# Kernel tuning notes

Measured on AMD Instinct MI355X. Metric: run time of the kernel, lower is better.

## Reference

```python
import jax, jax.numpy as jnp
import numpy as np

B, T, D, BOT = 4, 4096, 2048, 256


def setup_inputs() -> dict:
    key = jax.random.key(0)
    k1, k2, k3, k4 = jax.random.split(key, 4)
    return {
        "hdc_chars": jax.random.normal(k1, (B, T, D), dtype=jnp.float32),
        "decay_matrix": jax.random.uniform(k2, (B, T, T), dtype=jnp.float32),
        "Wq": jax.random.normal(k3, (BOT, D), dtype=jnp.float32) * (D ** -0.5),
        "bq": jnp.zeros((BOT,), dtype=jnp.float32),
        "Wk": jax.random.normal(k4, (BOT, D), dtype=jnp.float32) * (D ** -0.5),
        "bk": jnp.zeros((BOT,), dtype=jnp.float32),
    }


def reference(hdc_chars, decay_matrix, Wq, bq, Wk, bk):
    # hdc_chars: [B,T,D]; decay_matrix: [B,T,T]
    bot = Wq.shape[0]
    scale = bot ** -0.5
    q = hdc_chars @ Wq.T + bq          # [B,T,bot]
    k = hdc_chars @ Wk.T + bk          # [B,T,bot]
    scores = jnp.einsum("btc,bsc->bts", q, k) * scale  # [B,T,T]
    t = scores.shape[-1]
    i = jnp.arange(t)[:, None]
    j = jnp.arange(t)[None, :]
    allowed = j <= i - 4               # tril(diagonal=-4): blocks local echo
    scores = jnp.where(allowed, scores, jnp.float32(-65000.0))
    resonance = jax.nn.softmax(scores, axis=-1)
    combined = 0.7 * decay_matrix + 0.3 * resonance
    return combined @ hdc_chars        # [B,T,D]
```

## Files before the change

### kernel.cpp

```cpp
#include <hip/hip_runtime.h>
#include <hip/hip_bf16.h>

#define BB 4
#define TT 4096
#define DD 2048
#define BOTC 256

typedef __bf16 bf16;
typedef __attribute__((ext_vector_type(8))) __bf16 bf16x8;
typedef __attribute__((ext_vector_type(4))) float f32x4;

constexpr int BM = 128, BN = 128, BK = 32;

__device__ __forceinline__ void async16(const void* g, bf16* l) {
  __builtin_amdgcn_global_load_lds((const __attribute__((address_space(1))) void*)g,
                                   (__attribute__((address_space(3))) void*)l, 16, 0, 0);
}

template <int EPI>
__global__ __launch_bounds__(256) void gemm_bt(
    const bf16* __restrict__ A, const bf16* __restrict__ Bm, void* __restrict__ Cout,
    const float* __restrict__ bias, int M, int N, int K,
    long sAb, long sBb, long sCb, float scale) {
  const int b = blockIdx.z;
  const int m0 = blockIdx.y * BM;
  const int n0 = blockIdx.x * BN;
  const int tid = threadIdx.x;
  const int lane = tid & 63;
  const int w = tid >> 6;
  const int wm = (w >> 1) * 64;
  const int wn = (w & 1) * 64;

  if (EPI == 2 && n0 > m0) {
    bf16* C = (bf16*)Cout + (size_t)b * sCb;
    bf16 neg = (bf16)(-65000.0f);
    bf16x8 v8 = {neg, neg, neg, neg, neg, neg, neg, neg};
#pragma unroll
    for (int it = 0; it < 8; ++it) {
      int c = it * 256 + tid;
      int row = c >> 4, cc = c & 15;
      *(bf16x8*)(C + (size_t)(m0 + row) * N + n0 + cc * 8) = v8;
    }
    return;
  }

  __shared__ bf16 As[BM * BK];
  __shared__ bf16 Bs[BN * BK];

  f32x4 acc[4][4] = {};

  const bf16* Arow = A + (size_t)b * sAb + (size_t)m0 * K;
  const bf16* Brow = Bm + (size_t)b * sBb + (size_t)n0 * K;

  for (int k0 = 0; k0 < K; k0 += BK) {
#pragma unroll
    for (int j = 0; j < 2; ++j) {
      int c = j * 256 + tid;
      int row = c >> 2, kc = c & 3;
      async16(Arow + (size_t)row * K + k0 + kc * 8, As + c * 8);
      async16(Brow + (size_t)row * K + k0 + kc * 8, Bs + c * 8);
    }
    __syncthreads();
    bf16x8 af[4], bfr[4];
#pragma unroll
    for (int mi = 0; mi < 4; ++mi)
      af[mi] = *(const bf16x8*)(As + (wm + mi * 16 + (lane & 15)) * BK + (lane >> 4) * 8);
#pragma unroll
    for (int ni = 0; ni < 4; ++ni)
      bfr[ni] = *(const bf16x8*)(Bs + (wn + ni * 16 + (lane & 15)) * BK + (lane >> 4) * 8);
#pragma unroll
    for (int mi = 0; mi < 4; ++mi)
#pragma unroll
      for (int ni = 0; ni < 4; ++ni)
        acc[mi][ni] = __builtin_amdgcn_mfma_f32_16x16x32_bf16(af[mi], bfr[ni], acc[mi][ni], 0, 0, 0);
    __syncthreads();
  }

  const int lcol = lane & 15;
  const int lrow = (lane >> 4) * 4;

  if (EPI == 0) {
    float* C = (float*)Cout + (size_t)b * sCb;
#pragma unroll
    for (int mi = 0; mi < 4; ++mi) {
      int rbase = m0 + wm + mi * 16 + lrow;
#pragma unroll
      for (int ni = 0; ni < 4; ++ni) {
        int col = n0 + wn + ni * 16 + lcol;
#pragma unroll
        for (int r = 0; r < 4; ++r)
          C[(size_t)(rbase + r) * N + col] = acc[mi][ni][r];
      }
    }
  } else if (EPI == 1) {
    bf16* C = (bf16*)Cout + (size_t)b * sCb;
#pragma unroll
    for (int mi = 0; mi < 4; ++mi) {
      int rbase = m0 + wm + mi * 16 + lrow;
#pragma unroll
      for (int ni = 0; ni < 4; ++ni) {
        int col = n0 + wn + ni * 16 + lcol;
        float bv = bias[col];
#pragma unroll
        for (int r = 0; r < 4; ++r)
          C[(size_t)(rbase + r) * N + col] = (bf16)(acc[mi][ni][r] + bv);
      }
    }
  } else {
    bf16* C = (bf16*)Cout + (size_t)b * sCb;
#pragma unroll
    for (int mi = 0; mi < 4; ++mi) {
      int rbase = m0 + wm + mi * 16 + lrow;
#pragma unroll
      for (int ni = 0; ni < 4; ++ni) {
        int col = n0 + wn + ni * 16 + lcol;
#pragma unroll
        for (int r = 0; r < 4; ++r) {
          int i = rbase + r;
          float v = acc[mi][ni][r] * scale;
          if (col > i - 4) v = -65000.0f;
          C[(size_t)i * N + col] = (bf16)v;
        }
      }
    }
  }
}

__global__ __launch_bounds__(256) void conv_transpose(
    const float* __restrict__ hdc, bf16* __restrict__ hb, bf16* __restrict__ hT) {
  __shared__ float tile[32][33];
  int b = blockIdx.z;
  int d0 = blockIdx.x * 32, t0 = blockIdx.y * 32;
  int tx = threadIdx.x, ty = threadIdx.y;
  const float* src = hdc + (size_t)b * TT * DD;
  bf16* dstb = hb + (size_t)b * TT * DD;
  bf16* dstT = hT + (size_t)b * DD * TT;
#pragma unroll
  for (int rr = 0; rr < 32; rr += 8) {
    int r = ty + rr;
    float v = src[(size_t)(t0 + r) * DD + d0 + tx];
    tile[r][tx] = v;
    dstb[(size_t)(t0 + r) * DD + d0 + tx] = (bf16)v;
  }
  __syncthreads();
#pragma unroll
  for (int rr = 0; rr < 32; rr += 8) {
    int r = ty + rr;
    dstT[(size_t)(d0 + r) * TT + t0 + tx] = (bf16)tile[tx][r];
  }
}

__global__ __launch_bounds__(256) void conv_w(
    const float* __restrict__ Wq, const float* __restrict__ Wk,
    bf16* __restrict__ Wqb, bf16* __restrict__ Wkb) {
  int i = blockIdx.x * 256 + threadIdx.x;
  Wqb[i] = (bf16)Wq[i];
  Wkb[i] = (bf16)Wk[i];
}

__global__ __launch_bounds__(256) void softmax_combine(
    bf16* __restrict__ S, const float* __restrict__ decay) {
  int b = blockIdx.y, i = blockIdx.x;
  bf16* srow = S + ((size_t)b * TT + i) * TT;
  const float* drow = decay + ((size_t)b * TT + i) * TT;
  int t = threadIdx.x;
  int lane = t & 63, w = t >> 6;

  bf16x8 sv0 = *(const bf16x8*)(srow + (size_t)t * 8);
  bf16x8 sv1 = *(const bf16x8*)(srow + (size_t)(256 + t) * 8);
  float s[16];
#pragma unroll
  for (int e = 0; e < 8; ++e) { s[e] = (float)sv0[e]; s[8 + e] = (float)sv1[e]; }

  float m = s[0];
#pragma unroll
  for (int u = 1; u < 16; ++u) m = fmaxf(m, s[u]);
#pragma unroll
  for (int off = 32; off > 0; off >>= 1) m = fmaxf(m, __shfl_xor(m, off));
  __shared__ float redm[4], reds[4];
  if (lane == 0) redm[w] = m;
  __syncthreads();
  m = fmaxf(fmaxf(redm[0], redm[1]), fmaxf(redm[2], redm[3]));

  float p[16], sum = 0.f;
#pragma unroll
  for (int u = 0; u < 16; ++u) { p[u] = __expf(s[u] - m); sum += p[u]; }
#pragma unroll
  for (int off = 32; off > 0; off >>= 1) sum += __shfl_xor(sum, off);
  if (lane == 0) reds[w] = sum;
  __syncthreads();
  sum = reds[0] + reds[1] + reds[2] + reds[3];
  float inv = 0.3f / sum;

#pragma unroll
  for (int u = 0; u < 2; ++u) {
    int chunk = u * 256 + t;
    const float4* d4 = (const float4*)(drow + (size_t)chunk * 8);
    float4 da = d4[0], db = d4[1];
    bf16x8 o;
    o[0] = (bf16)(0.7f * da.x + p[u * 8 + 0] * inv);
    o[1] = (bf16)(0.7f * da.y + p[u * 8 + 1] * inv);
    o[2] = (bf16)(0.7f * da.z + p[u * 8 + 2] * inv);
    o[3] = (bf16)(0.7f * da.w + p[u * 8 + 3] * inv);
    o[4] = (bf16)(0.7f * db.x + p[u * 8 + 4] * inv);
    o[5] = (bf16)(0.7f * db.y + p[u * 8 + 5] * inv);
    o[6] = (bf16)(0.7f * db.z + p[u * 8 + 6] * inv);
    o[7] = (bf16)(0.7f * db.w + p[u * 8 + 7] * inv);
    *(bf16x8*)(srow + (size_t)chunk * 8) = o;
  }
}

extern "C" void kernel_launch(void* const* d_in, const int* in_sizes, int n_in,
                              void* d_out, int out_size, void* d_ws, size_t ws_size,
                              hipStream_t stream) {
  (void)in_sizes; (void)n_in; (void)out_size; (void)ws_size;
  const float* hdc = (const float*)d_in[0];
  const float* decay = (const float*)d_in[1];
  const float* Wq = (const float*)d_in[2];
  const float* bq = (const float*)d_in[3];
  const float* Wk = (const float*)d_in[4];
  const float* bk = (const float*)d_in[5];
  float* out = (float*)d_out;

  char* ws = (char*)d_ws;
  bf16* hdc_b = (bf16*)ws; ws += (size_t)BB * TT * DD * 2;
  bf16* hdcT  = (bf16*)ws; ws += (size_t)BB * TT * DD * 2;
  bf16* Wqb   = (bf16*)ws; ws += (size_t)BOTC * DD * 2;
  bf16* Wkb   = (bf16*)ws; ws += (size_t)BOTC * DD * 2;
  bf16* qb    = (bf16*)ws; ws += (size_t)BB * TT * BOTC * 2;
  bf16* kb    = (bf16*)ws; ws += (size_t)BB * TT * BOTC * 2;
  bf16* S     = (bf16*)ws; ws += (size_t)BB * TT * TT * 2;

  conv_transpose<<<dim3(DD / 32, TT / 32, BB), dim3(32, 8), 0, stream>>>(hdc, hdc_b, hdcT);
  conv_w<<<dim3(BOTC * DD / 256), 256, 0, stream>>>(Wq, Wk, Wqb, Wkb);

  gemm_bt<1><<<dim3(BOTC / BN, (BB * TT) / BM, 1), 256, 0, stream>>>(
      hdc_b, Wqb, qb, bq, BB * TT, BOTC, DD, 0, 0, 0, 1.0f);
  gemm_bt<1><<<dim3(BOTC / BN, (BB * TT) / BM, 1), 256, 0, stream>>>(
      hdc_b, Wkb, kb, bk, BB * TT, BOTC, DD, 0, 0, 0, 1.0f);

  gemm_bt<2><<<dim3(TT / BN, TT / BM, BB), 256, 0, stream>>>(
      qb, kb, S, nullptr, TT, TT, BOTC,
      (long)TT * BOTC, (long)TT * BOTC, (long)TT * TT, 0.0625f);

  softmax_combine<<<dim3(TT, BB), 256, 0, stream>>>(S, decay);

  gemm_bt<0><<<dim3(DD / BN, TT / BM, BB), 256, 0, stream>>>(
      S, hdcT, out, nullptr, TT, DD, TT,
      (long)TT * TT, (long)DD * TT, (long)TT * DD, 1.0f);
}
```

Before: 1.070 ms.

## Widen GEMM K-tile with XOR-swizzled LDS, fuse QK projection, skip masked score work

The GEMM K tile grows from 32 to 64 and the LDS layout is XOR-swizzled so fragment reads avoid bank conflicts. The Q and K projections are merged into one GEMM over a concatenated weight and bias buffer, writing an interleaved qk tensor read with leading-dimension strides. The score kernel no longer writes the masked upper tiles, and the softmax reads only the valid prefix of each row, handling fully masked rows as uniform. The transpose and conversion kernels are vectorized with 64x64 tiles. The changes aim to cut LDS stalls, kernel launches and memory traffic, at the cost of more complex indexing and larger LDS use per block.

```diff
diff --git a/kernel.cpp b/kernel.cpp
--- a/kernel.cpp
+++ b/kernel.cpp
@@ -7,10 +7,11 @@
 #define BOTC 256
 
 typedef __bf16 bf16;
+typedef __attribute__((ext_vector_type(4))) __bf16 bf16x4;
 typedef __attribute__((ext_vector_type(8))) __bf16 bf16x8;
 typedef __attribute__((ext_vector_type(4))) float f32x4;
 
-constexpr int BM = 128, BN = 128, BK = 32;
+constexpr int BM = 128, BN = 128, BK = 64;
 
 __device__ __forceinline__ void async16(const void* g, bf16* l) {
   __builtin_amdgcn_global_load_lds((const __attribute__((address_space(1))) void*)g,
@@ -20,7 +21,7 @@
 template <int EPI>
 __global__ __launch_bounds__(256) void gemm_bt(
     const bf16* __restrict__ A, const bf16* __restrict__ Bm, void* __restrict__ Cout,
-    const float* __restrict__ bias, int M, int N, int K,
+    const float* __restrict__ bias, int M, int N, int K, int ldA, int ldB,
     long sAb, long sBb, long sCb, float scale) {
   const int b = blockIdx.z;
   const int m0 = blockIdx.y * BM;
@@ -31,48 +32,50 @@
   const int wm = (w >> 1) * 64;
   const int wn = (w & 1) * 64;
 
-  if (EPI == 2 && n0 > m0) {
-    bf16* C = (bf16*)Cout + (size_t)b * sCb;
-    bf16 neg = (bf16)(-65000.0f);
-    bf16x8 v8 = {neg, neg, neg, neg, neg, neg, neg, neg};
-#pragma unroll
-    for (int it = 0; it < 8; ++it) {
-      int c = it * 256 + tid;
-      int row = c >> 4, cc = c & 15;
-      *(bf16x8*)(C + (size_t)(m0 + row) * N + n0 + cc * 8) = v8;
-    }
-    return;
-  }
+  if (EPI == 2 && n0 > m0) return;
 
   __shared__ bf16 As[BM * BK];
   __shared__ bf16 Bs[BN * BK];
 
   f32x4 acc[4][4] = {};
 
-  const bf16* Arow = A + (size_t)b * sAb + (size_t)m0 * K;
-  const bf16* Brow = Bm + (size_t)b * sBb + (size_t)n0 * K;
+  const bf16* Arow = A + (size_t)b * sAb + (size_t)m0 * ldA;
+  const bf16* Brow = Bm + (size_t)b * sBb + (size_t)n0 * ldB;
 
   for (int k0 = 0; k0 < K; k0 += BK) {
 #pragma unroll
-    for (int j = 0; j < 2; ++j) {
+    for (int j = 0; j < 4; ++j) {
       int c = j * 256 + tid;
-      int row = c >> 2, kc = c & 3;
-      async16(Arow + (size_t)row * K + k0 + kc * 8, As + c * 8);
-      async16(Brow + (size_t)row * K + k0 + kc * 8, Bs + c * 8);
+      int row = c >> 3, kc = c & 7;
+      int gk = kc ^ (row & 7);
+      async16(Arow + (size_t)row * ldA + k0 + gk * 8, As + (size_t)c * 8);
+      async16(Brow + (size_t)row * ldB + k0 + gk * 8, Bs + (size_t)c * 8);
     }
     __syncthreads();
-    bf16x8 af[4], bfr[4];
+    bf16x8 af[4][2], bfr[4][2];
 #pragma unroll
     for (int mi = 0; mi < 4; ++mi)
-      af[mi] = *(const bf16x8*)(As + (wm + mi * 16 + (lane & 15)) * BK + (lane >> 4) * 8);
+#pragma unroll
+      for (int kk = 0; kk < 2; ++kk) {
+        int row = wm + mi * 16 + (lane & 15);
+        int kc = kk * 4 + (lane >> 4);
+        af[mi][kk] = *(const bf16x8*)(As + ((size_t)row * 8 + (kc ^ (row & 7))) * 8);
+      }
 #pragma unroll
     for (int ni = 0; ni < 4; ++ni)
-      bfr[ni] = *(const bf16x8*)(Bs + (wn + ni * 16 + (lane & 15)) * BK + (lane >> 4) * 8);
-#pragma unroll
-    for (int mi = 0; mi < 4; ++mi)
-#pragma unroll
-      for (int ni = 0; ni < 4; ++ni)
-        acc[mi][ni] = __builtin_amdgcn_mfma_f32_16x16x32_bf16(af[mi], bfr[ni], acc[mi][ni], 0, 0, 0);
+#pragma unroll
+      for (int kk = 0; kk < 2; ++kk) {
+        int row = wn + ni * 16 + (lane & 15);
+        int kc = kk * 4 + (lane >> 4);
+        bfr[ni][kk] = *(const bf16x8*)(Bs + ((size_t)row * 8 + (kc ^ (row & 7))) * 8);
+      }
+#pragma unroll
+    for (int kk = 0; kk < 2; ++kk)
+#pragma unroll
+      for (int mi = 0; mi < 4; ++mi)
+#pragma unroll
+        for (int ni = 0; ni < 4; ++ni)
+          acc[mi][ni] = __builtin_amdgcn_mfma_f32_16x16x32_bf16(af[mi][kk], bfr[ni][kk], acc[mi][ni], 0, 0, 0);
     __syncthreads();
   }
 
@@ -128,34 +131,54 @@
 
 __global__ __launch_bounds__(256) void conv_transpose(
     const float* __restrict__ hdc, bf16* __restrict__ hb, bf16* __restrict__ hT) {
-  __shared__ float tile[32][33];
+  __shared__ float tile[64][65];
   int b = blockIdx.z;
-  int d0 = blockIdx.x * 32, t0 = blockIdx.y * 32;
-  int tx = threadIdx.x, ty = threadIdx.y;
+  int d0 = blockIdx.x * 64, t0 = blockIdx.y * 64;
+  int tid = threadIdx.x;
   const float* src = hdc + (size_t)b * TT * DD;
   bf16* dstb = hb + (size_t)b * TT * DD;
   bf16* dstT = hT + (size_t)b * DD * TT;
-#pragma unroll
-  for (int rr = 0; rr < 32; rr += 8) {
-    int r = ty + rr;
-    float v = src[(size_t)(t0 + r) * DD + d0 + tx];
-    tile[r][tx] = v;
-    dstb[(size_t)(t0 + r) * DD + d0 + tx] = (bf16)v;
+  int c4 = tid & 15, r0 = tid >> 4;
+#pragma unroll
+  for (int rr = 0; rr < 4; ++rr) {
+    int r = rr * 16 + r0;
+    float4 v = *(const float4*)(src + (size_t)(t0 + r) * DD + d0 + c4 * 4);
+    tile[r][c4 * 4 + 0] = v.x;
+    tile[r][c4 * 4 + 1] = v.y;
+    tile[r][c4 * 4 + 2] = v.z;
+    tile[r][c4 * 4 + 3] = v.w;
+    bf16x4 o;
+    o[0] = (bf16)v.x; o[1] = (bf16)v.y; o[2] = (bf16)v.z; o[3] = (bf16)v.w;
+    *(bf16x4*)(dstb + (size_t)(t0 + r) * DD + d0 + c4 * 4) = o;
   }
   __syncthreads();
-#pragma unroll
-  for (int rr = 0; rr < 32; rr += 8) {
-    int r = ty + rr;
-    dstT[(size_t)(d0 + r) * TT + t0 + tx] = (bf16)tile[tx][r];
+  int tc = tid & 7, dr0 = tid >> 3;
+#pragma unroll
+  for (int rr = 0; rr < 2; ++rr) {
+    int dr = rr * 32 + dr0;
+    bf16x8 o;
+#pragma unroll
+    for (int e = 0; e < 8; ++e) o[e] = (bf16)tile[tc * 8 + e][dr];
+    *(bf16x8*)(dstT + (size_t)(d0 + dr) * TT + t0 + tc * 8) = o;
   }
 }
 
 __global__ __launch_bounds__(256) void conv_w(
     const float* __restrict__ Wq, const float* __restrict__ Wk,
-    bf16* __restrict__ Wqb, bf16* __restrict__ Wkb) {
+    const float* __restrict__ bq, const float* __restrict__ bk,
+    bf16* __restrict__ Wqkb, float* __restrict__ bqk) {
   int i = blockIdx.x * 256 + threadIdx.x;
-  Wqb[i] = (bf16)Wq[i];
-  Wkb[i] = (bf16)Wk[i];
+  float4 q = *(const float4*)(Wq + (size_t)i * 4);
+  float4 k = *(const float4*)(Wk + (size_t)i * 4);
+  bf16x4 qo, ko;
+  qo[0] = (bf16)q.x; qo[1] = (bf16)q.y; qo[2] = (bf16)q.z; qo[3] = (bf16)q.w;
+  ko[0] = (bf16)k.x; ko[1] = (bf16)k.y; ko[2] = (bf16)k.z; ko[3] = (bf16)k.w;
+  *(bf16x4*)(Wqkb + (size_t)i * 4) = qo;
+  *(bf16x4*)(Wqkb + (size_t)BOTC * DD + (size_t)i * 4) = ko;
+  if (blockIdx.x == 0) {
+    bqk[threadIdx.x] = bq[threadIdx.x];
+    bqk[256 + threadIdx.x] = bk[threadIdx.x];
+  }
 }
 
 __global__ __launch_bounds__(256) void softmax_combine(
@@ -165,48 +188,81 @@
   const float* drow = decay + ((size_t)b * TT + i) * TT;
   int t = threadIdx.x;
   int lane = t & 63, w = t >> 6;
-
-  bf16x8 sv0 = *(const bf16x8*)(srow + (size_t)t * 8);
-  bf16x8 sv1 = *(const bf16x8*)(srow + (size_t)(256 + t) * 8);
-  float s[16];
-#pragma unroll
-  for (int e = 0; e < 8; ++e) { s[e] = (float)sv0[e]; s[8 + e] = (float)sv1[e]; }
-
-  float m = s[0];
-#pragma unroll
-  for (int u = 1; u < 16; ++u) m = fmaxf(m, s[u]);
-#pragma unroll
-  for (int off = 32; off > 0; off >>= 1) m = fmaxf(m, __shfl_xor(m, off));
-  __shared__ float redm[4], reds[4];
-  if (lane == 0) redm[w] = m;
-  __syncthreads();
-  m = fmaxf(fmaxf(redm[0], redm[1]), fmaxf(redm[2], redm[3]));
-
-  float p[16], sum = 0.f;
-#pragma unroll
-  for (int u = 0; u < 16; ++u) { p[u] = __expf(s[u] - m); sum += p[u]; }
-#pragma unroll
-  for (int off = 32; off > 0; off >>= 1) sum += __shfl_xor(sum, off);
-  if (lane == 0) reds[w] = sum;
-  __syncthreads();
-  sum = reds[0] + reds[1] + reds[2] + reds[3];
-  float inv = 0.3f / sum;
+  const int valid = i - 3;
+  const int nc = valid > 0 ? (valid + 7) >> 3 : 0;
+
+  float p[2][8];
+  float inv = 0.f, pc = 0.f;
+
+  if (valid > 0) {
+    float s[2][8];
+#pragma unroll
+    for (int u = 0; u < 2; ++u) {
+      int c = u * 256 + t;
+      if (c < nc) {
+        bf16x8 sv = *(const bf16x8*)(srow + (size_t)c * 8);
+#pragma unroll
+        for (int e = 0; e < 8; ++e) {
+          int j = c * 8 + e;
+          s[u][e] = j < valid ? (float)sv[e] : -INFINITY;
+        }
+      } else {
+#pragma unroll
+        for (int e = 0; e < 8; ++e) s[u][e] = -INFINITY;
+      }
+    }
+    float m = s[0][0];
+#pragma unroll
+    for (int u = 0; u < 2; ++u)
+#pragma unroll
+      for (int e = 0; e < 8; ++e) m = fmaxf(m, s[u][e]);
+#pragma unroll
+    for (int off = 32; off > 0; off >>= 1) m = fmaxf(m, __shfl_xor(m, off));
+    __shared__ float redm[4], reds[4];
+    if (lane == 0) redm[w] = m;
+    __syncthreads();
+    m = fmaxf(fmaxf(redm[0], redm[1]), fmaxf(redm[2], redm[3]));
+
+    float sum = 0.f;
+#pragma unroll
+    for (int u = 0; u < 2; ++u)
+#pragma unroll
+      for (int e = 0; e < 8; ++e) {
+        p[u][e] = __expf(s[u][e] - m);
+        sum += p[u][e];
+      }
+#pragma unroll
+    for (int off = 32; off > 0; off >>= 1) sum += __shfl_xor(sum, off);
+    if (lane == 0) reds[w] = sum;
+    __syncthreads();
+    sum = reds[0] + reds[1] + reds[2] + reds[3];
+    inv = 0.3f / sum;
+  } else {
+    pc = 0.3f / 4096.0f;
+#pragma unroll
+    for (int u = 0; u < 2; ++u)
+#pragma unroll
+      for (int e = 0; e < 8; ++e) p[u][e] = 0.f;
+  }
 
 #pragma unroll
   for (int u = 0; u < 2; ++u) {
-    int chunk = u * 256 + t;
-    const float4* d4 = (const float4*)(drow + (size_t)chunk * 8);
+    int c = u * 256 + t;
+    const float4* d4 = (const float4*)(drow + (size_t)c * 8);
     float4 da = d4[0], db = d4[1];
+    float pv[8];
+#pragma unroll
+    for (int e = 0; e < 8; ++e) pv[e] = p[u][e] * inv + pc;
     bf16x8 o;
-    o[0] = (bf16)(0.7f * da.x + p[u * 8 + 0] * inv);
-    o[1] = (bf16)(0.7f * da.y + p[u * 8 + 1] * inv);
-    o[2] = (bf16)(0.7f * da.z + p[u * 8 + 2] * inv);
-    o[3] = (bf16)(0.7f * da.w + p[u * 8 + 3] * inv);
-    o[4] = (bf16)(0.7f * db.x + p[u * 8 + 4] * inv);
-    o[5] = (bf16)(0.7f * db.y + p[u * 8 + 5] * inv);
-    o[6] = (bf16)(0.7f * db.z + p[u * 8 + 6] * inv);
-    o[7] = (bf16)(0.7f * db.w + p[u * 8 + 7] * inv);
-    *(bf16x8*)(srow + (size_t)chunk * 8) = o;
+    o[0] = (bf16)(0.7f * da.x + pv[0]);
+    o[1] = (bf16)(0.7f * da.y + pv[1]);
+    o[2] = (bf16)(0.7f * da.z + pv[2]);
+    o[3] = (bf16)(0.7f * da.w + pv[3]);
+    o[4] = (bf16)(0.7f * db.x + pv[4]);
+    o[5] = (bf16)(0.7f * db.y + pv[5]);
+    o[6] = (bf16)(0.7f * db.z + pv[6]);
+    o[7] = (bf16)(0.7f * db.w + pv[7]);
+    *(bf16x8*)(srow + (size_t)c * 8) = o;
   }
 }
 
@@ -225,27 +281,24 @@
   char* ws = (char*)d_ws;
   bf16* hdc_b = (bf16*)ws; ws += (size_t)BB * TT * DD * 2;
   bf16* hdcT  = (bf16*)ws; ws += (size_t)BB * TT * DD * 2;
-  bf16* Wqb   = (bf16*)ws; ws += (size_t)BOTC * DD * 2;
-  bf16* Wkb   = (bf16*)ws; ws += (size_t)BOTC * DD * 2;
-  bf16* qb    = (bf16*)ws; ws += (size_t)BB * TT * BOTC * 2;
-  bf16* kb    = (bf16*)ws; ws += (size_t)BB * TT * BOTC * 2;
+  bf16* Wqkb  = (bf16*)ws; ws += (size_t)2 * BOTC * DD * 2;
+  float* bqk  = (float*)ws; ws += 2 * BOTC * 4;
+  bf16* qk    = (bf16*)ws; ws += (size_t)BB * TT * 2 * BOTC * 2;
   bf16* S     = (bf16*)ws; ws += (size_t)BB * TT * TT * 2;
 
-  conv_transpose<<<dim3(DD / 32, TT / 32, BB), dim3(32, 8), 0, stream>>>(hdc, hdc_b, hdcT);
-  conv_w<<<dim3(BOTC * DD / 256), 256, 0, stream>>>(Wq, Wk, Wqb, Wkb);
-
-  gemm_bt<1><<<dim3(BOTC / BN, (BB * TT) / BM, 1), 256, 0, stream>>>(
-      hdc_b, Wqb, qb, bq, BB * TT, BOTC, DD, 0, 0, 0, 1.0f);
-  gemm_bt<1><<<dim3(BOTC / BN, (BB * TT) / BM, 1), 256, 0, stream>>>(
-      hdc_b, Wkb, kb, bk, BB * TT, BOTC, DD, 0, 0, 0, 1.0f);
+  conv_transpose<<<dim3(DD / 64, TT / 64, BB), 256, 0, stream>>>(hdc, hdc_b, hdcT);
+  conv_w<<<dim3(BOTC * DD / 1024), 256, 0, stream>>>(Wq, Wk, bq, bk, Wqkb, bqk);
+
+  gemm_bt<1><<<dim3((2 * BOTC) / BN, (BB * TT) / BM, 1), 256, 0, stream>>>(
+      hdc_b, Wqkb, qk, bqk, BB * TT, 2 * BOTC, DD, DD, DD, 0, 0, 0, 1.0f);
 
   gemm_bt<2><<<dim3(TT / BN, TT / BM, BB), 256, 0, stream>>>(
-      qb, kb, S, nullptr, TT, TT, BOTC,
-      (long)TT * BOTC, (long)TT * BOTC, (long)TT * TT, 0.0625f);
+      qk, qk + BOTC, S, nullptr, TT, TT, BOTC, 2 * BOTC, 2 * BOTC,
+      (long)TT * 2 * BOTC, (long)TT * 2 * BOTC, (long)TT * TT, 0.0625f);
 
   softmax_combine<<<dim3(TT, BB), 256, 0, stream>>>(S, decay);
 
   gemm_bt<0><<<dim3(DD / BN, TT / BM, BB), 256, 0, stream>>>(
-      S, hdcT, out, nullptr, TT, DD, TT,
+      S, hdcT, out, nullptr, TT, DD, TT, TT, TT,
       (long)TT * TT, (long)DD * TT, (long)TT * DD, 1.0f);
 }
```

After: 986.5 us. 1.09x faster.
